# Performance work log

Hardware: AMD Instinct MI355X
Metric: run time of the kernel (lower is better)

## Reference

```python
import jax, jax.numpy as jnp
import numpy as np

ALPHA = 0.001
BETA = 0.001
EPS = 1e-32


def setup_inputs() -> dict:
    key = jax.random.key(0)
    k1, k2, k3 = jax.random.split(key, 3)
    n = 16384
    log_h = jax.random.normal(k1, (n, 1), dtype=jnp.float32)
    durations = jax.random.uniform(k2, (n,), dtype=jnp.float32)  # positive observed times
    events = jnp.round(jax.random.uniform(k3, (n,), dtype=jnp.float32))  # 0/1 censoring indicator
    return {"log_h": log_h, "durations": durations, "events": events}


def reference(log_h, durations, events):
    n = durations.shape[0]
    # e = -(theta - log(Y + eps)), shape (n, 1)
    e = -(log_h - jnp.log(durations[:, None] + EPS))
    e_flat = e.reshape(-1)  # (n,)
    diff = e - e_flat  # (n, n): diff[i, j] = e_i - e_j
    masked = jnp.abs(diff * (diff <= 0))  # = relu(e_j - e_i)
    loss = jnp.sum(masked * events[:, None]) * (1.0 / (n * n))
    penalty_1 = ALPHA * jnp.sum(e ** 2) / n
    penalty_2 = BETA * jnp.sum(log_h ** 2) / n
    return loss + penalty_1 + penalty_2
```

## Files before the change

kernel.cpp:

```cpp
#include <hip/hip_runtime.h>
#include <math.h>

#define ALPHA 0.001f
#define BETA  0.001f
#define EPS   1e-32f

constexpr int BLOCK  = 256;
constexpr int ITILE  = 8;
constexpr int JCHUNK = 256;

typedef _Float16 f16x2 __attribute__((ext_vector_type(2)));

__device__ __forceinline__ float dot2acc(f16x2 a, float c) {
#if __has_builtin(__builtin_amdgcn_fdot2)
    const f16x2 one2 = {(_Float16)1.0f, (_Float16)1.0f};
    return __builtin_amdgcn_fdot2(a, one2, c, false);
#else
    return c + (float)a.x + (float)a.y;
#endif
}

__global__ __launch_bounds__(BLOCK) void pair_fused_kernel(
        const float* __restrict__ log_h,
        const float* __restrict__ dur,
        const float* __restrict__ events,
        float* __restrict__ lossp,
        float* __restrict__ penp,
        int nib, int n) {
    __shared__ alignas(16) _Float16 se[JCHUNK];
    const int tid = threadIdx.x;
    const int bid = blockIdx.x;
    const int bx  = bid % nib;
    const int by  = bid / nib;

    const int i0 = bx * (BLOCK * ITILE);
    const int iv = i0 / 4 + tid * 2;
    float4 lh4a = ((const float4*)log_h)[iv],  lh4b = ((const float4*)log_h)[iv + 1];
    float4 du4a = ((const float4*)dur)[iv],    du4b = ((const float4*)dur)[iv + 1];
    float4 ev4a = ((const float4*)events)[iv], ev4b = ((const float4*)events)[iv + 1];

    {
        int j = by * JCHUNK + tid;
        float ejf = __logf(dur[j] + EPS) - log_h[j];
        se[tid] = (_Float16)ejf;
    }

    float acc[ITILE], ev[ITILE], eih[ITILE];
    f16x2 ei2[ITILE];
    float pen = 0.f;
    {
        const float lhs[8] = {lh4a.x, lh4a.y, lh4a.z, lh4a.w,
                              lh4b.x, lh4b.y, lh4b.z, lh4b.w};
        const float dus[8] = {du4a.x, du4a.y, du4a.z, du4a.w,
                              du4b.x, du4b.y, du4b.z, du4b.w};
        const float evs[8] = {ev4a.x, ev4a.y, ev4a.z, ev4a.w,
                              ev4b.x, ev4b.y, ev4b.z, ev4b.w};
        #pragma unroll
        for (int u = 0; u < ITILE; ++u) {
            float lh = lhs[u];
            float ei = __logf(dus[u] + EPS) - lh;
            ev[u] = evs[u];
            _Float16 h = (_Float16)ei;
            ei2[u] = (f16x2){h, h};
            eih[u] = (float)h;
            pen += ALPHA * ei * ei + BETA * lh * lh;
            acc[u] = 0.f;
        }
    }
    __syncthreads();

    const uint4* sev = (const uint4*)se;
    #pragma unroll 4
    for (int k = 0; k < JCHUNK / 8; ++k) {
        uint4 raw = sev[k];
        f16x2 h0 = __builtin_bit_cast(f16x2, raw.x);
        f16x2 h1 = __builtin_bit_cast(f16x2, raw.y);
        f16x2 h2 = __builtin_bit_cast(f16x2, raw.z);
        f16x2 h3 = __builtin_bit_cast(f16x2, raw.w);
        #pragma unroll
        for (int u = 0; u < ITILE; ++u) {
            acc[u] = dot2acc(__builtin_elementwise_max(h0, ei2[u]), acc[u]);
            acc[u] = dot2acc(__builtin_elementwise_max(h1, ei2[u]), acc[u]);
            acc[u] = dot2acc(__builtin_elementwise_max(h2, ei2[u]), acc[u]);
            acc[u] = dot2acc(__builtin_elementwise_max(h3, ei2[u]), acc[u]);
        }
    }

    float loss = 0.f;
    #pragma unroll
    for (int u = 0; u < ITILE; ++u)
        loss += ev[u] * (acc[u] - (float)JCHUNK * eih[u]);

    for (int off = 32; off; off >>= 1) {
        loss += __shfl_down(loss, off);
        pen  += __shfl_down(pen, off);
    }
    __shared__ float wl[BLOCK / 64], wp[BLOCK / 64];
    if ((tid & 63) == 0) { wl[tid >> 6] = loss; wp[tid >> 6] = pen; }
    __syncthreads();
    if (tid == 0) {
        float tl = 0.f, tp = 0.f;
        for (int w = 0; w < BLOCK / 64; ++w) { tl += wl[w]; tp += wp[w]; }
        lossp[by * nib + bx] = tl;
        if (by == 0) penp[bx] = tp;
    }
}

__global__ void finalize_kernel(const float* __restrict__ lossp, int nloss,
                                const float* __restrict__ penp, int npen,
                                float* __restrict__ out, int n) {
    const int tid = threadIdx.x;
    const float invn  = 1.0f / (float)n;
    const float invn2 = invn * invn;
    float v = 0.f;
    for (int k = tid; k < nloss; k += BLOCK) v += lossp[k] * invn2;
    for (int k = tid; k < npen;  k += BLOCK) v += penp[k] * invn;
    for (int off = 32; off; off >>= 1) v += __shfl_down(v, off);
    __shared__ float ws[BLOCK / 64];
    if ((tid & 63) == 0) ws[tid >> 6] = v;
    __syncthreads();
    if (tid == 0) {
        float t = 0.f;
        for (int w = 0; w < BLOCK / 64; ++w) t += ws[w];
        out[0] = t;
    }
}

extern "C" void kernel_launch(void* const* d_in, const int* in_sizes, int n_in,
                              void* d_out, int out_size, void* d_ws, size_t ws_size,
                              hipStream_t stream) {
    const float* log_h  = (const float*)d_in[0];
    const float* dur    = (const float*)d_in[1];
    const float* events = (const float*)d_in[2];
    float* out = (float*)d_out;
    const int n = in_sizes[1];

    const int nib = n / (BLOCK * ITILE);
    const int njc = n / JCHUNK;
    const int nblocks = nib * njc;

    float* lossp = (float*)d_ws;
    float* penp  = lossp + nblocks;

    pair_fused_kernel<<<nblocks, BLOCK, 0, stream>>>(log_h, dur, events,
                                                     lossp, penp, nib, n);
    finalize_kernel<<<1, BLOCK, 0, stream>>>(lossp, nblocks, penp, nib, out, n);
}
```

Measured before the change: 18.84 us.

## Compact event-positive rows per block and skip censored rows in pair loop

Each block runs a prefix scan over the event flags and compacts only the rows with events into a shared-memory list. The pairwise max/dot2 loop then iterates over ceil(C/256) rows per thread instead of a fixed 8, with a templated switch over K. Roughly half the events are zero, so this targets about half the pair arithmetic. The cost is an extra prefix scan, a shared-memory scatter, a second barrier and a padding sentinel for the unused slots. Padded slots hold 60000, so max() returns the pad for every j and the acc - 256*pad term cancels to zero.

```diff
diff --git a/kernel.cpp b/kernel.cpp
--- a/kernel.cpp
+++ b/kernel.cpp
@@ -8,6 +8,7 @@
 constexpr int BLOCK  = 256;
 constexpr int ITILE  = 8;
 constexpr int JCHUNK = 256;
+#define PADF 60000.0f
 
 typedef _Float16 f16x2 __attribute__((ext_vector_type(2)));
 
@@ -18,6 +19,43 @@
 #else
     return c + (float)a.x + (float)a.y;
 #endif
+}
+
+template<int K>
+__device__ __forceinline__ float inner_loop(const _Float16* __restrict__ se,
+                                            const _Float16* __restrict__ ce,
+                                            int tid, int C) {
+    float acc[K], eih[K];
+    f16x2 ei2[K];
+    #pragma unroll
+    for (int u = 0; u < K; ++u) {
+        int r = u * BLOCK + tid;
+        _Float16 h = (r < C) ? ce[r] : (_Float16)PADF;
+        ei2[u] = (f16x2){h, h};
+        eih[u] = (float)h;
+        acc[u] = 0.f;
+    }
+    const uint4* sev = (const uint4*)se;
+    #pragma unroll 4
+    for (int k = 0; k < JCHUNK / 8; ++k) {
+        uint4 raw = sev[k];
+        f16x2 h0 = __builtin_bit_cast(f16x2, raw.x);
+        f16x2 h1 = __builtin_bit_cast(f16x2, raw.y);
+        f16x2 h2 = __builtin_bit_cast(f16x2, raw.z);
+        f16x2 h3 = __builtin_bit_cast(f16x2, raw.w);
+        #pragma unroll
+        for (int u = 0; u < K; ++u) {
+            acc[u] = dot2acc(__builtin_elementwise_max(h0, ei2[u]), acc[u]);
+            acc[u] = dot2acc(__builtin_elementwise_max(h1, ei2[u]), acc[u]);
+            acc[u] = dot2acc(__builtin_elementwise_max(h2, ei2[u]), acc[u]);
+            acc[u] = dot2acc(__builtin_elementwise_max(h3, ei2[u]), acc[u]);
+        }
+    }
+    float loss = 0.f;
+    #pragma unroll
+    for (int u = 0; u < K; ++u)
+        loss += acc[u] - (float)JCHUNK * eih[u];
+    return loss;
 }
 
 __global__ __launch_bounds__(BLOCK) void pair_fused_kernel(
@@ -28,6 +66,8 @@
         float* __restrict__ penp,
         int nib, int n) {
     __shared__ alignas(16) _Float16 se[JCHUNK];
+    __shared__ alignas(16) _Float16 ce[BLOCK * ITILE];
+    __shared__ int wt[BLOCK / 64];
     const int tid = threadIdx.x;
     const int bid = blockIdx.x;
     const int bx  = bid % nib;
@@ -45,9 +85,10 @@
         se[tid] = (_Float16)ejf;
     }
 
-    float acc[ITILE], ev[ITILE], eih[ITILE];
-    f16x2 ei2[ITILE];
+    _Float16 h[ITILE];
+    bool flag[ITILE];
     float pen = 0.f;
+    int cnt = 0;
     {
         const float lhs[8] = {lh4a.x, lh4a.y, lh4a.z, lh4a.w,
                               lh4b.x, lh4b.y, lh4b.z, lh4b.w};
@@ -59,37 +100,49 @@
         for (int u = 0; u < ITILE; ++u) {
             float lh = lhs[u];
             float ei = __logf(dus[u] + EPS) - lh;
-            ev[u] = evs[u];
-            _Float16 h = (_Float16)ei;
-            ei2[u] = (f16x2){h, h};
-            eih[u] = (float)h;
+            h[u] = (_Float16)ei;
+            flag[u] = (evs[u] != 0.0f);
+            cnt += flag[u] ? 1 : 0;
             pen += ALPHA * ei * ei + BETA * lh * lh;
-            acc[u] = 0.f;
         }
     }
-    __syncthreads();
-
-    const uint4* sev = (const uint4*)se;
-    #pragma unroll 4
-    for (int k = 0; k < JCHUNK / 8; ++k) {
-        uint4 raw = sev[k];
-        f16x2 h0 = __builtin_bit_cast(f16x2, raw.x);
-        f16x2 h1 = __builtin_bit_cast(f16x2, raw.y);
-        f16x2 h2 = __builtin_bit_cast(f16x2, raw.z);
-        f16x2 h3 = __builtin_bit_cast(f16x2, raw.w);
+
+    int inc = cnt;
+    #pragma unroll
+    for (int off = 1; off < 64; off <<= 1) {
+        int y = __shfl_up(inc, off);
+        if ((tid & 63) >= off) inc += y;
+    }
+    if ((tid & 63) == 63) wt[tid >> 6] = inc;
+    __syncthreads();
+    int wbase = 0;
+    #pragma unroll
+    for (int w = 0; w < BLOCK / 64; ++w)
+        wbase += (w < (tid >> 6)) ? wt[w] : 0;
+    const int C = wt[0] + wt[1] + wt[2] + wt[3];
+
+    {
+        int p = wbase + inc - cnt;
         #pragma unroll
         for (int u = 0; u < ITILE; ++u) {
-            acc[u] = dot2acc(__builtin_elementwise_max(h0, ei2[u]), acc[u]);
-            acc[u] = dot2acc(__builtin_elementwise_max(h1, ei2[u]), acc[u]);
-            acc[u] = dot2acc(__builtin_elementwise_max(h2, ei2[u]), acc[u]);
-            acc[u] = dot2acc(__builtin_elementwise_max(h3, ei2[u]), acc[u]);
+            if (flag[u]) { ce[p] = h[u]; ++p; }
         }
     }
-
+    __syncthreads();
+
+    const int K = (C + BLOCK - 1) >> 8;
     float loss = 0.f;
-    #pragma unroll
-    for (int u = 0; u < ITILE; ++u)
-        loss += ev[u] * (acc[u] - (float)JCHUNK * eih[u]);
+    switch (K) {
+        case 1: loss = inner_loop<1>(se, ce, tid, C); break;
+        case 2: loss = inner_loop<2>(se, ce, tid, C); break;
+        case 3: loss = inner_loop<3>(se, ce, tid, C); break;
+        case 4: loss = inner_loop<4>(se, ce, tid, C); break;
+        case 5: loss = inner_loop<5>(se, ce, tid, C); break;
+        case 6: loss = inner_loop<6>(se, ce, tid, C); break;
+        case 7: loss = inner_loop<7>(se, ce, tid, C); break;
+        case 8: loss = inner_loop<8>(se, ce, tid, C); break;
+        default: break;
+    }
 
     for (int off = 32; off; off >>= 1) {
         loss += __shfl_down(loss, off);
```

Measured after the change: 15.89 us (median of 2 runs). 15.7% less time.
